# Performance work log

Hardware: AMD Instinct MI355X
Metric: run time of the kernel (lower is better)

The kernel has to match this reference:

```python
import jax, jax.numpy as jnp
import numpy as np

B, S, D = 4, 2048, 512
H = 8
DEPTH = D // H  # 64


def setup_inputs() -> dict:
    key = jax.random.key(0)
    ks = jax.random.split(key, 6)
    scale = 1.0 / np.sqrt(D)
    return {
        "x": jax.random.normal(ks[0], (B, S, D), dtype=jnp.float32),
        "y": jax.random.normal(ks[1], (B, S, D), dtype=jnp.float32),
        "W_q": jax.random.normal(ks[2], (D, D), dtype=jnp.float32) * scale,
        "W_k": jax.random.normal(ks[3], (D, D), dtype=jnp.float32) * scale,
        "W_v": jax.random.normal(ks[4], (D, D), dtype=jnp.float32) * scale,
        "W_o": jax.random.normal(ks[5], (D, D), dtype=jnp.float32) * scale,
    }


def _split_heads(t):
    # [B, S, D] -> [B, H, S, DEPTH]
    b, s, _ = t.shape
    return t.reshape(b, s, H, DEPTH).transpose(0, 2, 1, 3)


def reference(x, y, W_q, W_k, W_v, W_o):
    q = _split_heads(x @ W_q) * (DEPTH ** -0.5)   # [B,H,Sq,d]
    k = _split_heads(y @ W_k)                      # [B,H,Sk,d]
    v = _split_heads(y @ W_v)                      # [B,H,Sk,d]
    logits = jnp.einsum("bhqd,bhkd->bhqk", q, k)   # [B,H,Sq,Sk]
    weights = jax.nn.softmax(logits, axis=-1)
    attn = jnp.einsum("bhqk,bhkd->bhqd", weights, v)  # [B,H,Sq,d]
    attn = attn.transpose(0, 2, 1, 3).reshape(x.shape[0], x.shape[1], D)
    return attn @ W_o
```

## Files before the change

### kernel.cpp

```cpp
#include <hip/hip_runtime.h>
#include <hip/hip_bf16.h>
#include <math.h>
#include <stdint.h>

#define NB 4
#define NS 2048
#define ND 512
#define NH 8
#define DEP 64

typedef __attribute__((ext_vector_type(8))) short bf16x8;
typedef __attribute__((ext_vector_type(4))) short bf16x4;
typedef __attribute__((ext_vector_type(4))) float f32x4;

#define QSCALE 0.18033688011112042f

__device__ __forceinline__ short f2b(float f) {
  unsigned u = __float_as_uint(f);
  u += 0x7FFF + ((u >> 16) & 1);
  return (short)(u >> 16);
}
__device__ __forceinline__ unsigned pk2(float a, float b) {
  union { __hip_bfloat162 h; unsigned u; } c;
  c.h = __float22bfloat162_rn(float2{a, b});
  return c.u;
}
__device__ __forceinline__ void dma16(const void* g, void* l) {
  __builtin_amdgcn_global_load_lds(
      (const __attribute__((address_space(1))) void*)g,
      (__attribute__((address_space(3))) void*)l, 16, 0, 0);
}

__global__ __launch_bounds__(256) void prep(
    const float* __restrict__ x, const float* __restrict__ y,
    const float* __restrict__ W0, const float* __restrict__ W1,
    const float* __restrict__ W2, const float* __restrict__ W3,
    short* __restrict__ xb, short* __restrict__ yb, short* __restrict__ T0,
    short* __restrict__ T1, short* __restrict__ T2, short* __restrict__ T3) {
  const int t = threadIdx.x;
  if (blockIdx.y < 2) {
    const float* src = blockIdx.y ? y : x;
    short* dst = blockIdx.y ? yb : xb;
    size_t i = ((size_t)blockIdx.x * 256 + t) * 4;
    float4 v = *(const float4*)(src + i);
    bf16x4 o;
    o[0] = f2b(v.x); o[1] = f2b(v.y); o[2] = f2b(v.z); o[3] = f2b(v.w);
    *(bf16x4*)(dst + i) = o;
    return;
  }
  const int bx = blockIdx.x;
  if (bx >= 256) return;
  const int wj = bx >> 6, rem = bx & 63;
  const float* W = wj == 0 ? W0 : wj == 1 ? W1 : wj == 2 ? W2 : W3;
  short* T = wj == 0 ? T0 : wj == 1 ? T1 : wj == 2 ? T2 : T3;
  __shared__ float tile[64][65];
  const int k0 = (rem >> 3) * 64, n0 = (rem & 7) * 64;
#pragma unroll
  for (int i = 0; i < 4; ++i) {
    int r = (t >> 4) + i * 16;
    int c = (t & 15) * 4;
    float4 v = *(const float4*)&W[(size_t)(k0 + r) * ND + n0 + c];
    tile[r][c] = v.x; tile[r][c + 1] = v.y;
    tile[r][c + 2] = v.z; tile[r][c + 3] = v.w;
  }
  __syncthreads();
#pragma unroll
  for (int i = 0; i < 4; ++i) {
    int n = (t >> 4) + i * 16;
    int kc = (t & 15) * 4;
    bf16x4 o;
#pragma unroll
    for (int j = 0; j < 4; ++j) o[j] = f2b(tile[kc + j][n]);
    *(bf16x4*)&T[(size_t)(n0 + n) * ND + k0 + kc] = o;
  }
}

__device__ __forceinline__ void gemm128(const short* __restrict__ A,
                                        const short* __restrict__ Bt,
                                        short* __restrict__ Cout, int mode,
                                        float alpha) {
  __shared__ short As[128 * 64];
  __shared__ short Bs[128 * 64];
  const int t = threadIdx.x;
  const int wave = t >> 6, lane = t & 63;
  const int m = lane & 15, quad = lane >> 4;
  const int m0 = blockIdx.y * 128, n0 = blockIdx.x * 128;
  const int mh = (wave >> 1) * 64, nh = (wave & 1) * 64;
  const int r8 = lane >> 3;
  const int c8 = (lane & 7) ^ r8;
  const int mx7 = m & 7;
  f32x4 acc[4][4];
#pragma unroll
  for (int i = 0; i < 4; ++i)
#pragma unroll
    for (int j = 0; j < 4; ++j) acc[i][j] = (f32x4){0.f, 0.f, 0.f, 0.f};

  for (int k0 = 0; k0 < ND; k0 += 64) {
    __syncthreads();
#pragma unroll
    for (int i = 0; i < 4; ++i) {
      int row = i * 32 + wave * 8 + r8;
      dma16(A + (size_t)(m0 + row) * ND + k0 + c8 * 8,
            As + (i * 256 + wave * 64) * 8);
      dma16(Bt + (size_t)(n0 + row) * ND + k0 + c8 * 8,
            Bs + (i * 256 + wave * 64) * 8);
    }
    __syncthreads();
    bf16x8 af[4][2], bf[4][2];
#pragma unroll
    for (int mt = 0; mt < 4; ++mt)
#pragma unroll
      for (int kc = 0; kc < 2; ++kc)
        af[mt][kc] = *(const bf16x8*)(As + (mh + mt * 16 + m) * 64 +
                                      ((kc * 4 + quad) ^ mx7) * 8);
#pragma unroll
    for (int nt = 0; nt < 4; ++nt)
#pragma unroll
      for (int kc = 0; kc < 2; ++kc)
        bf[nt][kc] = *(const bf16x8*)(Bs + (nh + nt * 16 + m) * 64 +
                                      ((kc * 4 + quad) ^ mx7) * 8);
#pragma unroll
    for (int mt = 0; mt < 4; ++mt)
#pragma unroll
      for (int nt = 0; nt < 4; ++nt)
#pragma unroll
        for (int kc = 0; kc < 2; ++kc)
          acc[mt][nt] = __builtin_amdgcn_mfma_f32_16x16x32_bf16(
              af[mt][kc], bf[nt][kc], acc[mt][nt], 0, 0, 0);
  }
  if (mode == 2) {
#pragma unroll
    for (int mt = 0; mt < 4; ++mt)
#pragma unroll
      for (int nt = 0; nt < 4; ++nt) {
        int row0 = m0 + mh + mt * 16 + quad * 4;
        int col = n0 + nh + nt * 16 + m;
        int b_ = row0 >> 11, s_ = row0 & (NS - 1);
        int h_ = col >> 6, d_ = col & (DEP - 1);
        uint2 p;
        p.x = pk2(acc[mt][nt][0] * alpha, acc[mt][nt][1] * alpha);
        p.y = pk2(acc[mt][nt][2] * alpha, acc[mt][nt][3] * alpha);
        *(uint2*)(Cout + (size_t)((b_ * NH + h_) * DEP + d_) * NS + s_) = p;
      }
  } else {
#pragma unroll
    for (int mt = 0; mt < 4; ++mt)
#pragma unroll
      for (int nt = 0; nt < 4; ++nt)
#pragma unroll
        for (int r = 0; r < 4; ++r) {
          int row = m0 + mh + mt * 16 + quad * 4 + r;
          int col = n0 + nh + nt * 16 + m;
          Cout[(size_t)row * ND + col] = f2b(acc[mt][nt][r] * alpha);
        }
  }
}

__global__ __launch_bounds__(256) void qkv_gemm(
    const short* __restrict__ xb, const short* __restrict__ yb,
    const short* __restrict__ Wqt, const short* __restrict__ Wkt,
    const short* __restrict__ Wvt, short* __restrict__ Qb,
    short* __restrict__ Kb, short* __restrict__ Vtb) {
  if (blockIdx.z == 0)
    gemm128(xb, Wqt, Qb, 1, QSCALE);
  else if (blockIdx.z == 1)
    gemm128(yb, Wkt, Kb, 1, 1.0f);
  else
    gemm128(yb, Wvt, Vtb, 2, 1.0f);
}

__global__ __launch_bounds__(256) void out_gemm(const short* __restrict__ A,
                                                const short* __restrict__ Bt,
                                                float* __restrict__ Cout) {
  __shared__ short As[2][128 * 64];
  __shared__ short Bs[2][64 * 64];
  const int t = threadIdx.x;
  const int wave = t >> 6, lane = t & 63;
  const int m = lane & 15, quad = lane >> 4;
  const int m0 = blockIdx.y * 128, n0 = blockIdx.x * 64;
  const int mh = (wave >> 1) * 64, nh = (wave & 1) * 32;
  const int r8 = lane >> 3;
  const int c8 = (lane & 7) ^ r8;
  const int mx7 = m & 7;
  f32x4 acc[4][2];
#pragma unroll
  for (int i = 0; i < 4; ++i)
#pragma unroll
    for (int j = 0; j < 2; ++j) acc[i][j] = (f32x4){0.f, 0.f, 0.f, 0.f};

#pragma unroll
  for (int i = 0; i < 4; ++i)
    dma16(A + (size_t)(m0 + i * 32 + wave * 8 + r8) * ND + c8 * 8,
          As[0] + (i * 256 + wave * 64) * 8);
#pragma unroll
  for (int i = 0; i < 2; ++i)
    dma16(Bt + (size_t)(n0 + i * 32 + wave * 8 + r8) * ND + c8 * 8,
          Bs[0] + (i * 256 + wave * 64) * 8);

  int buf = 0;
  for (int k0 = 0; k0 < ND; k0 += 64, buf ^= 1) {
    __syncthreads();
    if (k0 + 64 < ND) {
#pragma unroll
      for (int i = 0; i < 4; ++i)
        dma16(A + (size_t)(m0 + i * 32 + wave * 8 + r8) * ND + k0 + 64 + c8 * 8,
              As[buf ^ 1] + (i * 256 + wave * 64) * 8);
#pragma unroll
      for (int i = 0; i < 2; ++i)
        dma16(Bt + (size_t)(n0 + i * 32 + wave * 8 + r8) * ND + k0 + 64 +
                  c8 * 8,
              Bs[buf ^ 1] + (i * 256 + wave * 64) * 8);
    }
    bf16x8 af[4][2], bf[2][2];
#pragma unroll
    for (int mt = 0; mt < 4; ++mt)
#pragma unroll
      for (int kc = 0; kc < 2; ++kc)
        af[mt][kc] = *(const bf16x8*)(As[buf] + (mh + mt * 16 + m) * 64 +
                                      ((kc * 4 + quad) ^ mx7) * 8);
#pragma unroll
    for (int nt = 0; nt < 2; ++nt)
#pragma unroll
      for (int kc = 0; kc < 2; ++kc)
        bf[nt][kc] = *(const bf16x8*)(Bs[buf] + (nh + nt * 16 + m) * 64 +
                                      ((kc * 4 + quad) ^ mx7) * 8);
#pragma unroll
    for (int mt = 0; mt < 4; ++mt)
#pragma unroll
      for (int nt = 0; nt < 2; ++nt)
#pragma unroll
        for (int kc = 0; kc < 2; ++kc)
          acc[mt][nt] = __builtin_amdgcn_mfma_f32_16x16x32_bf16(
              af[mt][kc], bf[nt][kc], acc[mt][nt], 0, 0, 0);
  }
#pragma unroll
  for (int mt = 0; mt < 4; ++mt)
#pragma unroll
    for (int nt = 0; nt < 2; ++nt)
#pragma unroll
      for (int r = 0; r < 4; ++r) {
        int row = m0 + mh + mt * 16 + quad * 4 + r;
        int col = n0 + nh + nt * 16 + m;
        Cout[(size_t)row * ND + col] = acc[mt][nt][r];
      }
}

__global__ __launch_bounds__(256) void attn_mfma(const short* __restrict__ Qb,
                                                 const short* __restrict__ Kb,
                                                 const short* __restrict__ Vtb,
                                                 short* __restrict__ Ob) {
  __shared__ short Ks[2][64 * 64];
  __shared__ short Vts[2][64 * 64];
  __shared__ short Pt[64 * 64];
  const int t = threadIdx.x;
  const int wave = t >> 6, lane = t & 63;
  const int m = lane & 15, quad = lane >> 4;
  const int bh = blockIdx.y, b = bh >> 3, h = bh & 7;
  const int q0 = blockIdx.x * 64;
  const int wq = wave * 16;
  const size_t rowb = (size_t)b * NS;
  const short* Vtbase = Vtb + (size_t)(bh * DEP) * NS;
  const int r8 = lane >> 3;
  const int c8 = (lane & 7) ^ r8;
  const int mx7 = m & 7;

  bf16x8 qf[2];
#pragma unroll
  for (int kc = 0; kc < 2; ++kc)
    qf[kc] = *(const bf16x8*)(Qb + (rowb + q0 + wq + m) * ND + h * DEP +
                              kc * 32 + quad * 8);

  float l_ = 0.0f;
  f32x4 Ot[4];
#pragma unroll
  for (int mt = 0; mt < 4; ++mt) Ot[mt] = (f32x4){0.f, 0.f, 0.f, 0.f};

#pragma unroll
  for (int i = 0; i < 2; ++i) {
    int row = i * 32 + wave * 8 + r8;
    dma16(Kb + (rowb + row) * ND + h * DEP + c8 * 8,
          Ks[0] + (i * 256 + wave * 64) * 8);
    dma16(Vtbase + (size_t)row * NS + c8 * 8,
          Vts[0] + (i * 256 + wave * 64) * 8);
  }

  int buf = 0;
  for (int kv0 = 0; kv0 < NS; kv0 += 64, buf ^= 1) {
    __syncthreads();
    if (kv0 + 64 < NS) {
#pragma unroll
      for (int i = 0; i < 2; ++i) {
        int row = i * 32 + wave * 8 + r8;
        dma16(Kb + (rowb + kv0 + 64 + row) * ND + h * DEP + c8 * 8,
              Ks[buf ^ 1] + (i * 256 + wave * 64) * 8);
        dma16(Vtbase + (size_t)row * NS + kv0 + 64 + c8 * 8,
              Vts[buf ^ 1] + (i * 256 + wave * 64) * 8);
      }
    }

    f32x4 St[4];
#pragma unroll
    for (int mt = 0; mt < 4; ++mt) St[mt] = (f32x4){0.f, 0.f, 0.f, 0.f};
#pragma unroll
    for (int mt = 0; mt < 4; ++mt)
#pragma unroll
      for (int kc = 0; kc < 2; ++kc) {
        bf16x8 kf = *(const bf16x8*)(Ks[buf] + (mt * 16 + m) * 64 +
                                     ((kc * 4 + quad) ^ mx7) * 8);
        St[mt] = __builtin_amdgcn_mfma_f32_16x16x32_bf16(kf, qf[kc], St[mt],
                                                         0, 0, 0);
      }

    float rs = 0.0f;
#pragma unroll
    for (int mt = 0; mt < 4; ++mt) {
      float p0 = __builtin_amdgcn_exp2f(St[mt][0]);
      float p1 = __builtin_amdgcn_exp2f(St[mt][1]);
      float p2 = __builtin_amdgcn_exp2f(St[mt][2]);
      float p3 = __builtin_amdgcn_exp2f(St[mt][3]);
      rs += (p0 + p1) + (p2 + p3);
      uint2 pk;
      pk.x = pk2(p0, p1);
      pk.y = pk2(p2, p3);
      *(uint2*)(Pt + (wq + m) * 64 + ((mt * 2 + (quad >> 1)) ^ mx7) * 8 +
                (quad & 1) * 4) = pk;
    }
    l_ += rs;

#pragma unroll
    for (int kc = 0; kc < 2; ++kc) {
      bf16x8 pf = *(const bf16x8*)(Pt + (wq + m) * 64 +
                                   ((kc * 4 + quad) ^ mx7) * 8);
#pragma unroll
      for (int mt = 0; mt < 4; ++mt) {
        bf16x8 vf = *(const bf16x8*)(Vts[buf] + (mt * 16 + m) * 64 +
                                     ((kc * 4 + quad) ^ mx7) * 8);
        Ot[mt] = __builtin_amdgcn_mfma_f32_16x16x32_bf16(vf, pf, Ot[mt],
                                                         0, 0, 0);
      }
    }
  }

  l_ += __shfl_xor(l_, 16, 64);
  l_ += __shfl_xor(l_, 32, 64);
  float linv = 1.0f / l_;
  size_t row = rowb + q0 + wq + m;
#pragma unroll
  for (int mt = 0; mt < 4; ++mt)
#pragma unroll
    for (int r = 0; r < 4; ++r)
      Ob[row * ND + h * DEP + mt * 16 + quad * 4 + r] = f2b(Ot[mt][r] * linv);
}

extern "C" void kernel_launch(void* const* d_in, const int* in_sizes, int n_in,
                              void* d_out, int out_size, void* d_ws,
                              size_t ws_size, hipStream_t stream) {
  const float* x = (const float*)d_in[0];
  const float* y = (const float*)d_in[1];
  const float* Wq = (const float*)d_in[2];
  const float* Wk = (const float*)d_in[3];
  const float* Wv = (const float*)d_in[4];
  const float* Wo = (const float*)d_in[5];
  float* out = (float*)d_out;

  const size_t mat = (size_t)NB * NS * ND;
  const size_t wsz = (size_t)ND * ND;
  short* xb = (short*)d_ws;
  short* yb = xb + mat;
  short* Wqt = yb + mat;
  short* Wkt = Wqt + wsz;
  short* Wvt = Wkt + wsz;
  short* Wot = Wvt + wsz;
  short* Qb = Wot + wsz;
  short* Kb = Qb + mat;
  short* Vtb = Kb + mat;
  short* attnb = xb;

  prep<<<dim3(mat / 1024, 3), 256, 0, stream>>>(x, y, Wq, Wk, Wv, Wo, xb, yb,
                                                Wqt, Wkt, Wvt, Wot);
  qkv_gemm<<<dim3(ND / 128, (NB * NS) / 128, 3), 256, 0, stream>>>(
      xb, yb, Wqt, Wkt, Wvt, Qb, Kb, Vtb);
  attn_mfma<<<dim3(NS / 64, NB * NH), 256, 0, stream>>>(Qb, Kb, Vtb, attnb);
  out_gemm<<<dim3(ND / 64, (NB * NS) / 128), 256, 0, stream>>>(attnb, Wot,
                                                               out);
}
```

Baseline: 192.0 us.

## Use 32x32x16 MFMA in attention with register-resident P via permlane32_swap

Rewrites the attention kernel to use 32x32x16 bf16 MFMA tiles, so each wave handles 32 query rows and each block 128 queries, which halves the grid. The softmax probabilities are repacked in registers with permlane32_swap instead of being written to and read back from a shared-memory P tile. This removes LDS round-trips for P and reuses each K/V tile across more queries, at the cost of more accumulator registers and fewer blocks in flight. The output is also written as packed bf16 stores instead of scalar stores.

Measured after the change: 190.1 us. No clear change (-1.0%).

```diff
diff --git a/kernel.cpp b/kernel.cpp
--- a/kernel.cpp
+++ b/kernel.cpp
@@ -12,6 +12,7 @@
 typedef __attribute__((ext_vector_type(8))) short bf16x8;
 typedef __attribute__((ext_vector_type(4))) short bf16x4;
 typedef __attribute__((ext_vector_type(4))) float f32x4;
+typedef __attribute__((ext_vector_type(16))) float f32x16;
 
 #define QSCALE 0.18033688011112042f
 
@@ -251,29 +252,29 @@
                                                  short* __restrict__ Ob) {
   __shared__ short Ks[2][64 * 64];
   __shared__ short Vts[2][64 * 64];
-  __shared__ short Pt[64 * 64];
   const int t = threadIdx.x;
   const int wave = t >> 6, lane = t & 63;
-  const int m = lane & 15, quad = lane >> 4;
+  const int l31 = lane & 31, hi = lane >> 5;
+  const int sw = lane & 7;
   const int bh = blockIdx.y, b = bh >> 3, h = bh & 7;
-  const int q0 = blockIdx.x * 64;
-  const int wq = wave * 16;
+  const int q0 = blockIdx.x * 128 + wave * 32;
   const size_t rowb = (size_t)b * NS;
   const short* Vtbase = Vtb + (size_t)(bh * DEP) * NS;
   const int r8 = lane >> 3;
   const int c8 = (lane & 7) ^ r8;
-  const int mx7 = m & 7;
-
-  bf16x8 qf[2];
-#pragma unroll
-  for (int kc = 0; kc < 2; ++kc)
-    qf[kc] = *(const bf16x8*)(Qb + (rowb + q0 + wq + m) * ND + h * DEP +
-                              kc * 32 + quad * 8);
+
+  bf16x8 qf[4];
+#pragma unroll
+  for (int dc = 0; dc < 4; ++dc)
+    qf[dc] = *(const bf16x8*)(Qb + (rowb + q0 + l31) * ND + h * DEP + dc * 16 +
+                              hi * 8);
 
   float l_ = 0.0f;
-  f32x4 Ot[4];
-#pragma unroll
-  for (int mt = 0; mt < 4; ++mt) Ot[mt] = (f32x4){0.f, 0.f, 0.f, 0.f};
+  f32x16 Ot[2];
+#pragma unroll
+  for (int dt = 0; dt < 2; ++dt)
+#pragma unroll
+    for (int i = 0; i < 16; ++i) Ot[dt][i] = 0.f;
 
 #pragma unroll
   for (int i = 0; i < 2; ++i) {
@@ -298,58 +299,67 @@
       }
     }
 
-    f32x4 St[4];
-#pragma unroll
-    for (int mt = 0; mt < 4; ++mt) St[mt] = (f32x4){0.f, 0.f, 0.f, 0.f};
-#pragma unroll
-    for (int mt = 0; mt < 4; ++mt)
-#pragma unroll
-      for (int kc = 0; kc < 2; ++kc) {
-        bf16x8 kf = *(const bf16x8*)(Ks[buf] + (mt * 16 + m) * 64 +
-                                     ((kc * 4 + quad) ^ mx7) * 8);
-        St[mt] = __builtin_amdgcn_mfma_f32_16x16x32_bf16(kf, qf[kc], St[mt],
+    f32x16 St[2];
+#pragma unroll
+    for (int kt = 0; kt < 2; ++kt)
+#pragma unroll
+      for (int i = 0; i < 16; ++i) St[kt][i] = 0.f;
+#pragma unroll
+    for (int kt = 0; kt < 2; ++kt)
+#pragma unroll
+      for (int dc = 0; dc < 4; ++dc) {
+        bf16x8 kf = *(const bf16x8*)(&Ks[buf][(kt * 32 + l31) * 64 +
+                                              ((dc * 2 + hi) ^ sw) * 8]);
+        St[kt] = __builtin_amdgcn_mfma_f32_32x32x16_bf16(kf, qf[dc], St[kt],
                                                          0, 0, 0);
       }
 
-    float rs = 0.0f;
-#pragma unroll
-    for (int mt = 0; mt < 4; ++mt) {
-      float p0 = __builtin_amdgcn_exp2f(St[mt][0]);
-      float p1 = __builtin_amdgcn_exp2f(St[mt][1]);
-      float p2 = __builtin_amdgcn_exp2f(St[mt][2]);
-      float p3 = __builtin_amdgcn_exp2f(St[mt][3]);
-      rs += (p0 + p1) + (p2 + p3);
-      uint2 pk;
-      pk.x = pk2(p0, p1);
-      pk.y = pk2(p2, p3);
-      *(uint2*)(Pt + (wq + m) * 64 + ((mt * 2 + (quad >> 1)) ^ mx7) * 8 +
-                (quad & 1) * 4) = pk;
+    bf16x8 pf[4];
+    float rs = 0.f;
+#pragma unroll
+    for (int s = 0; s < 4; ++s) {
+      const int kt = s >> 1, base = (s & 1) * 8;
+      float E[8];
+#pragma unroll
+      for (int j = 0; j < 8; ++j) {
+        E[j] = __builtin_amdgcn_exp2f(St[kt][base + j]);
+        rs += E[j];
+      }
+      unsigned A0 = pk2(E[0], E[1]), A1 = pk2(E[2], E[3]);
+      unsigned A2 = pk2(E[4], E[5]), A3 = pk2(E[6], E[7]);
+      auto r02 =
+          __builtin_amdgcn_permlane32_swap((int)A0, (int)A2, false, false);
+      auto r13 =
+          __builtin_amdgcn_permlane32_swap((int)A1, (int)A3, false, false);
+      union { bf16x8 v; int u[4]; } pu;
+      pu.u[0] = r02[0]; pu.u[1] = r13[0]; pu.u[2] = r02[1]; pu.u[3] = r13[1];
+      pf[s] = pu.v;
     }
     l_ += rs;
 
 #pragma unroll
-    for (int kc = 0; kc < 2; ++kc) {
-      bf16x8 pf = *(const bf16x8*)(Pt + (wq + m) * 64 +
-                                   ((kc * 4 + quad) ^ mx7) * 8);
-#pragma unroll
-      for (int mt = 0; mt < 4; ++mt) {
-        bf16x8 vf = *(const bf16x8*)(Vts[buf] + (mt * 16 + m) * 64 +
-                                     ((kc * 4 + quad) ^ mx7) * 8);
-        Ot[mt] = __builtin_amdgcn_mfma_f32_16x16x32_bf16(vf, pf, Ot[mt],
+    for (int dt = 0; dt < 2; ++dt)
+#pragma unroll
+      for (int s = 0; s < 4; ++s) {
+        bf16x8 vf = *(const bf16x8*)(&Vts[buf][(dt * 32 + l31) * 64 +
+                                               ((s * 2 + hi) ^ sw) * 8]);
+        Ot[dt] = __builtin_amdgcn_mfma_f32_32x32x16_bf16(vf, pf[s], Ot[dt],
                                                          0, 0, 0);
       }
-    }
-  }
-
-  l_ += __shfl_xor(l_, 16, 64);
+  }
+
   l_ += __shfl_xor(l_, 32, 64);
   float linv = 1.0f / l_;
-  size_t row = rowb + q0 + wq + m;
-#pragma unroll
-  for (int mt = 0; mt < 4; ++mt)
-#pragma unroll
-    for (int r = 0; r < 4; ++r)
-      Ob[row * ND + h * DEP + mt * 16 + quad * 4 + r] = f2b(Ot[mt][r] * linv);
+  size_t row = rowb + q0 + l31;
+#pragma unroll
+  for (int dt = 0; dt < 2; ++dt)
+#pragma unroll
+    for (int g = 0; g < 4; ++g) {
+      uint2 pk;
+      pk.x = pk2(Ot[dt][g * 4 + 0] * linv, Ot[dt][g * 4 + 1] * linv);
+      pk.y = pk2(Ot[dt][g * 4 + 2] * linv, Ot[dt][g * 4 + 3] * linv);
+      *(uint2*)(Ob + row * ND + h * DEP + dt * 32 + g * 8 + hi * 4) = pk;
+    }
 }
 
 extern "C" void kernel_launch(void* const* d_in, const int* in_sizes, int n_in,
@@ -380,7 +390,7 @@
                                                 Wqt, Wkt, Wvt, Wot);
   qkv_gemm<<<dim3(ND / 128, (NB * NS) / 128, 3), 256, 0, stream>>>(
       xb, yb, Wqt, Wkt, Wvt, Qb, Kb, Vtb);
-  attn_mfma<<<dim3(NS / 64, NB * NH), 256, 0, stream>>>(Qb, Kb, Vtb, attnb);
+  attn_mfma<<<dim3(NS / 128, NB * NH), 256, 0, stream>>>(Qb, Kb, Vtb, attnb);
   out_gemm<<<dim3(ND / 64, (NB * NS) / 128), 256, 0, stream>>>(attnb, Wot,
                                                                out);
 }
```
